# Kernel optimization log

Hardware: AMD Instinct MI355X
Metric: run time of the kernel (lower is better)

## Reference

```python
import jax, jax.numpy as jnp
import numpy as np
import math

V, T, D_POI, D_OUT = 200000, 512, 256, 512
D_IN = D_POI + 4
D_HID = D_POI + 100


def setup_inputs() -> dict:
    key = jax.random.key(0)
    ks = jax.random.split(key, 12)
    s = 0.02
    return {
        "prev_poi_idx": jax.random.randint(ks[0], (T,), 0, V),
        "prev_time_frac": jax.random.uniform(ks[1], (T,), jnp.float32),
        "poi_final_emb": jax.random.normal(ks[2], (V, D_POI), jnp.float32),
        "poi_latlon_deg": jax.random.uniform(ks[3], (V, 2), jnp.float32) * 90.0,
        "ln_w": jnp.ones((D_IN,), jnp.float32),
        "ln_b": jnp.zeros((D_IN,), jnp.float32),
        "w1": jax.random.normal(ks[4], (D_IN, D_HID), jnp.float32) * s,
        "b1": jnp.zeros((D_HID,), jnp.float32),
        "w2": jax.random.normal(ks[5], (D_HID, D_POI), jnp.float32) * s,
        "b2": jnp.zeros((D_POI,), jnp.float32),
        "w_ih": jax.random.normal(ks[6], (3 * D_OUT, D_POI), jnp.float32) * s,
        "w_hh": jax.random.normal(ks[7], (3 * D_OUT, D_OUT), jnp.float32) * s,
        "b_ih": jnp.zeros((3 * D_OUT,), jnp.float32),
        "b_hh": jnp.zeros((3 * D_OUT,), jnp.float32),
        "q": jax.random.normal(ks[8], (D_OUT,), jnp.float32),
        "log_lam": jnp.array(0.0, jnp.float32),  # log(recency_lambda=1.0)
    }


def _haversine_km(lat1, lon1, lat2, lon2, eps=1e-12):
    dlat = (lat2 - lat1) * 0.5
    dlon = (lon2 - lon1) * 0.5
    a = jnp.sin(dlat) ** 2 + jnp.clip(jnp.cos(lat1), -1, 1) * jnp.clip(jnp.cos(lat2), -1, 1) * jnp.sin(dlon) ** 2
    c = 2.0 * jnp.arctan2(jnp.sqrt(jnp.clip(a, 0, 1)), jnp.sqrt(jnp.clip(1 - a, eps, 1)))
    return 6371.0088 * c


def _forward(prev_poi_idx, prev_time_frac, poi_final_emb, poi_latlon_deg,
             ln_w, ln_b, w1, b1, w2, b2, w_ih, w_hh, b_ih, b_hh, q, log_lam):
    Tn = prev_poi_idx.shape[0]
    poi_emb = poi_final_emb[prev_poi_idx]                       # (T, d_poi)
    t = jnp.clip(prev_time_frac, 0.0, 1.0)
    sin_t = jnp.sin(2.0 * math.pi * t)
    cos_t = jnp.cos(2.0 * math.pi * t)
    dif = jnp.mod(t[1:] - t[:-1], 1.0) * 24.0
    dt_h = jnp.concatenate([jnp.zeros((1,), t.dtype), dif])
    # _poi_radians is under no_grad in torch
    latlon = jax.lax.stop_gradient(poi_latlon_deg[prev_poi_idx])
    lat = jnp.deg2rad(jnp.clip(latlon[:, 0], -90, 90))
    lon = jnp.deg2rad(jnp.clip(latlon[:, 1], -180, 180))
    dd = _haversine_km(lat[:-1], lon[:-1], lat[1:], lon[1:])
    dd_km = jnp.concatenate([jnp.zeros((1,), dd.dtype), dd])
    feat = jnp.stack([sin_t, cos_t, jnp.log1p(dt_h), jnp.log1p(dd_km)], axis=-1)  # (T, 4)
    x = jnp.concatenate([poi_emb, feat], axis=-1)               # (T, d_poi+4)
    # fuse: LayerNorm -> Linear -> GELU -> (Dropout eval=id) -> Linear
    mu = jnp.mean(x, axis=-1, keepdims=True)
    var = jnp.mean((x - mu) ** 2, axis=-1, keepdims=True)
    x = (x - mu) * jax.lax.rsqrt(var + 1e-5) * ln_w + ln_b
    x = jax.nn.gelu(x @ w1 + b1, approximate=False) @ w2 + b2   # (T, d_poi)
    # GRU (single layer, unidirectional), torch gate order r,z,n
    gi_all = x @ w_ih.T + b_ih                                  # (T, 3H)
    def step(h, gi):
        gh = h @ w_hh.T + b_hh
        gi_r, gi_z, gi_n = jnp.split(gi, 3)
        gh_r, gh_z, gh_n = jnp.split(gh, 3)
        r = jax.nn.sigmoid(gi_r + gh_r)
        z = jax.nn.sigmoid(gi_z + gh_z)
        n = jnp.tanh(gi_n + r * gh_n)
        h_new = (1.0 - z) * n + z * h
        return h_new, h_new
    h0 = jnp.zeros((D_OUT,), x.dtype)
    _, hs = jax.lax.scan(step, h0, gi_all)                      # (T, d_out)
    D = hs.shape[-1]
    score = hs @ (q[:D] / jnp.sqrt(jnp.asarray(D, hs.dtype)))
    age = jnp.arange(Tn, dtype=hs.dtype)
    lam = jnp.maximum(jnp.exp(log_lam), 1e-4)
    score = score - lam * (Tn - 1 - age)
    attn = jax.nn.softmax(score, axis=0)
    summary = jnp.sum(attn[:, None] * hs, axis=0, keepdims=True)  # (1, d_out)
    return summary, attn


def reference(prev_poi_idx, prev_time_frac, poi_final_emb, poi_latlon_deg,
              ln_w, ln_b, w1, b1, w2, b2, w_ih, w_hh, b_ih, b_hh, q, log_lam):
    return _forward(prev_poi_idx, prev_time_frac, poi_final_emb, poi_latlon_deg,
                    ln_w, ln_b, w1, b1, w2, b2, w_ih, w_hh, b_ih, b_hh, q, log_lam)
```

## Files before the change

### kernel.cpp

```cpp
#include <hip/hip_runtime.h>
#include <hip/hip_cooperative_groups.h>
#include <math.h>

namespace cg = cooperative_groups;

#define TT 512
#define DPOI 256
#define DIN 260
#define DHID 356
#define DOUTD 512
#define G3 1536

#define GB 32
#define HU (DOUTD / GB)
#define NR (3 * HU)

__global__ void feat_kernel(const int* __restrict__ idx, const float* __restrict__ timef,
                            const float* __restrict__ latlon, float* __restrict__ feat) {
    int i = threadIdx.x;
    if (i >= TT) return;
    float t = fminf(fmaxf(timef[i], 0.f), 1.f);
    const float TWO_PI = 6.28318530717958647692f;
    float s = sinf(TWO_PI * t);
    float c = cosf(TWO_PI * t);
    float dt_h = 0.f, dd = 0.f;
    if (i > 0) {
        float tp = fminf(fmaxf(timef[i - 1], 0.f), 1.f);
        float d = t - tp;
        d = d - floorf(d);
        dt_h = d * 24.f;
        int i0 = idx[i - 1], i1 = idx[i];
        float la0 = latlon[2 * (size_t)i0], lo0 = latlon[2 * (size_t)i0 + 1];
        float la1 = latlon[2 * (size_t)i1], lo1 = latlon[2 * (size_t)i1 + 1];
        const float D2R = 0.01745329251994329577f;
        float lat1 = fminf(fmaxf(la0, -90.f), 90.f) * D2R;
        float lon1 = fminf(fmaxf(lo0, -180.f), 180.f) * D2R;
        float lat2 = fminf(fmaxf(la1, -90.f), 90.f) * D2R;
        float lon2 = fminf(fmaxf(lo1, -180.f), 180.f) * D2R;
        float dlat = (lat2 - lat1) * 0.5f, dlon = (lon2 - lon1) * 0.5f;
        float sdlat = sinf(dlat), sdlon = sinf(dlon);
        float a = sdlat * sdlat +
                  fminf(fmaxf(cosf(lat1), -1.f), 1.f) * fminf(fmaxf(cosf(lat2), -1.f), 1.f) * sdlon * sdlon;
        float aa = fminf(fmaxf(a, 0.f), 1.f);
        float bb = fminf(fmaxf(1.f - a, 1e-12f), 1.f);
        float cc = 2.f * atan2f(sqrtf(aa), sqrtf(bb));
        dd = 6371.0088f * cc;
    }
    feat[4 * i + 0] = s;
    feat[4 * i + 1] = c;
    feat[4 * i + 2] = log1pf(dt_h);
    feat[4 * i + 3] = log1pf(dd);
}

__global__ void ln_kernel(const int* __restrict__ idx, const float* __restrict__ emb,
                          const float* __restrict__ feat, const float* __restrict__ lnw,
                          const float* __restrict__ lnb, float* __restrict__ xn) {
    int t = blockIdx.x;
    int tid = threadIdx.x;
    int wave = tid >> 6, lane = tid & 63;
    const float* row = emb + (size_t)idx[t] * DPOI;
    float v0 = row[tid];
    float v1 = (tid < 4) ? feat[4 * t + tid] : 0.f;

    __shared__ float red[4];
    __shared__ float mu_s, rs_s;

    float s = v0 + v1;
    for (int o = 32; o; o >>= 1) s += __shfl_down(s, o, 64);
    if (lane == 0) red[wave] = s;
    __syncthreads();
    if (tid == 0) mu_s = (red[0] + red[1] + red[2] + red[3]) * (1.f / 260.f);
    __syncthreads();
    float mu = mu_s;
    float d0 = v0 - mu;
    float d1 = (tid < 4) ? (v1 - mu) : 0.f;
    float sq = d0 * d0 + d1 * d1;
    for (int o = 32; o; o >>= 1) sq += __shfl_down(sq, o, 64);
    __syncthreads();
    if (lane == 0) red[wave] = sq;
    __syncthreads();
    if (tid == 0) {
        float var = (red[0] + red[1] + red[2] + red[3]) * (1.f / 260.f);
        rs_s = rsqrtf(var + 1e-5f);
    }
    __syncthreads();
    float rs = rs_s;
    xn[t * DIN + tid] = d0 * rs * lnw[tid] + lnb[tid];
    if (tid < 4)
        xn[t * DIN + 256 + tid] = d1 * rs * lnw[256 + tid] + lnb[256 + tid];
}

__global__ void mlp1_kernel(const float* __restrict__ xn, const float* __restrict__ w1,
                            const float* __restrict__ b1, float* __restrict__ h1) {
    int t = blockIdx.x, j = threadIdx.x;
    __shared__ float xl[DIN];
    for (int k = threadIdx.x; k < DIN; k += blockDim.x) xl[k] = xn[t * DIN + k];
    __syncthreads();
    if (j < DHID) {
        float acc = b1[j];
        #pragma unroll 4
        for (int k = 0; k < DIN; ++k) acc = fmaf(xl[k], w1[k * DHID + j], acc);
        float g = 0.5f * acc * (1.f + erff(acc * 0.70710678118654752440f));
        h1[t * DHID + j] = g;
    }
}

__global__ void mlp2_kernel(const float* __restrict__ h1, const float* __restrict__ w2,
                            const float* __restrict__ b2, float* __restrict__ x2) {
    int t = blockIdx.x, j = threadIdx.x;
    __shared__ float xl[DHID];
    for (int k = threadIdx.x; k < DHID; k += blockDim.x) xl[k] = h1[t * DHID + k];
    __syncthreads();
    float acc = b2[j];
    #pragma unroll 4
    for (int k = 0; k < DHID; ++k) acc = fmaf(xl[k], w2[k * DPOI + j], acc);
    x2[t * DPOI + j] = acc;
}

__global__ void gi_kernel(const float* __restrict__ x2, const float* __restrict__ wih,
                          const float* __restrict__ bih, float* __restrict__ gi) {
    int t = blockIdx.x;
    int tid = threadIdx.x;
    int wave = tid >> 6, lane = tid & 63;
    float4 xv = ((const float4*)(x2 + (size_t)t * DPOI))[lane];
    for (int r = wave; r < G3; r += 4) {
        float4 wv = ((const float4*)(wih + (size_t)r * DPOI))[lane];
        float s = xv.x * wv.x + xv.y * wv.y + xv.z * wv.z + xv.w * wv.w;
        for (int o = 32; o; o >>= 1) s += __shfl_down(s, o, 64);
        if (lane == 0) gi[(size_t)t * G3 + r] = s + bih[r];
    }
}

__global__ void zero_kernel(uint4* __restrict__ p, int n16) {
    int i = blockIdx.x * blockDim.x + threadIdx.x;
    int stride = gridDim.x * blockDim.x;
    uint4 z; z.x = 0u; z.y = 0u; z.z = 0u; z.w = 0u;
    for (; i < n16; i += stride) p[i] = z;
}

__global__ __launch_bounds__(1024)
void gru_tag_kernel(const float* __restrict__ gi, const float* __restrict__ whh,
                    const float* __restrict__ bhh, float* __restrict__ hs,
                    unsigned long long* __restrict__ hcomm) {
    __shared__ unsigned short w[NR][DOUTD];
    __shared__ float hprev[DOUTD];
    __shared__ float gsum[NR];
    __shared__ float bl[NR];

    int b = blockIdx.x;
    int tid = threadIdx.x;
    int wave = tid >> 6, lane = tid & 63;
    int jbase = b * HU;

    unsigned short* wl = &w[0][0];
    for (int e = tid; e < NR * DOUTD; e += 1024) {
        int rr = e >> 9, k = e & 511;
        int g = rr >> 4, jj = rr & 15;
        float v = whh[(size_t)(g * DOUTD + jbase + jj) * DOUTD + k];
        unsigned int u = __float_as_uint(v);
        u += 0x7fffu + ((u >> 16) & 1u);
        int kk = (k < 256) ? (((k >> 2) << 3) | (k & 3))
                           : ((((k - 256) >> 2) << 3) | 4 | (k & 3));
        wl[(rr << 9) + kk] = (unsigned short)(u >> 16);
    }
    if (tid < NR) {
        int g = tid >> 4, jj = tid & 15;
        bl[tid] = bhh[g * DOUTD + jbase + jj];
    }
    if (tid < DOUTD) hprev[tid] = 0.f;
    __syncthreads();

    const float4* hp4 = (const float4*)hprev;
    long budget = 2L * 1000 * 1000;

    float gir = 0.f, giz = 0.f, gin = 0.f, hreg = 0.f;
    if (tid < HU) {
        int j = jbase + tid;
        gir = gi[j];
        giz = gi[DOUTD + j];
        gin = gi[2 * DOUTD + j];
    }

    for (int s = 0; s < TT; ++s) {
        if (s > 0) {
            if (lane < 32) {
                int v = (wave << 5) + lane;
                bool own = (v >> 4) == b;
                const unsigned long long* ap = hcomm + (size_t)(s - 1) * DOUTD + v;
                unsigned long long p = 0;
                bool ok = own;
                while (!__all(ok)) {
                    if (!ok) {
                        p = __hip_atomic_load(ap, __ATOMIC_RELAXED,
                                              __HIP_MEMORY_SCOPE_AGENT);
                        ok = ((unsigned)(p >> 32) == (unsigned)s);
                    }
                    if (--budget < 0) break;
                }
                if (!own) hprev[v] = __uint_as_float((unsigned)p);
            }
            __syncthreads();
        }

        float4 ha = hp4[lane];
        float4 hb = hp4[64 + lane];
        #pragma unroll
        for (int rv = 0; rv < 3; ++rv) {
            int rr = wave * 3 + rv;
            uint4 wv = *(const uint4*)(wl + (rr << 9) + (lane << 3));
            float acc;
            acc = __uint_as_float(wv.x << 16) * ha.x;
            acc = fmaf(__uint_as_float(wv.x & 0xffff0000u), ha.y, acc);
            acc = fmaf(__uint_as_float(wv.y << 16), ha.z, acc);
            acc = fmaf(__uint_as_float(wv.y & 0xffff0000u), ha.w, acc);
            acc = fmaf(__uint_as_float(wv.z << 16), hb.x, acc);
            acc = fmaf(__uint_as_float(wv.z & 0xffff0000u), hb.y, acc);
            acc = fmaf(__uint_as_float(wv.w << 16), hb.z, acc);
            acc = fmaf(__uint_as_float(wv.w & 0xffff0000u), hb.w, acc);
            for (int o = 32; o; o >>= 1) acc += __shfl_down(acc, o, 64);
            if (lane == 0) gsum[rr] = acc + bl[rr];
        }
        __syncthreads();

        if (tid < HU) {
            int j = jbase + tid;
            float gr  = gir + gsum[tid];
            float gz  = giz + gsum[HU + tid];
            float ghn = gsum[2 * HU + tid];
            float r = 1.f / (1.f + expf(-gr));
            float z = 1.f / (1.f + expf(-gz));
            float n = tanhf(gin + r * ghn);
            float hn = (1.f - z) * n + z * hreg;
            hreg = hn;
            hs[(size_t)s * DOUTD + j] = hn;
            unsigned long long pay = ((unsigned long long)(unsigned)(s + 1) << 32) |
                                     (unsigned long long)__float_as_uint(hn);
            __hip_atomic_store(&hcomm[(size_t)s * DOUTD + j], pay,
                               __ATOMIC_RELAXED, __HIP_MEMORY_SCOPE_AGENT);
            hprev[j] = hn;
            if (s + 1 < TT) {
                const float* gn = gi + (size_t)(s + 1) * G3;
                gir = gn[j]; giz = gn[DOUTD + j]; gin = gn[2 * DOUTD + j];
            }
        }
    }
}

__global__ void attn_kernel(const float* __restrict__ hs, const float* __restrict__ q,
                            const float* __restrict__ log_lam, float* __restrict__ out) {
    int tid = threadIdx.x;
    int wave = tid >> 6, lane = tid & 63;
    __shared__ float sc[TT];
    __shared__ float at[TT];
    __shared__ float red[8];
    __shared__ float red2[8];
    __shared__ float denom_s, mx_s;

    const float qscale = 0.04419417382415921757f;
    for (int r = wave; r < TT; r += 8) {
        float acc = 0.f;
        #pragma unroll
        for (int m = 0; m < 8; ++m) {
            int k = lane + 64 * m;
            acc = fmaf(hs[(size_t)r * DOUTD + k], q[k], acc);
        }
        for (int o = 32; o; o >>= 1) acc += __shfl_down(acc, o, 64);
        if (lane == 0) sc[r] = acc * qscale;
    }
    __syncthreads();
    float lam = fmaxf(expf(log_lam[0]), 1e-4f);
    float s_i = sc[tid] - lam * (float)(TT - 1 - tid);

    float mval = s_i;
    for (int o = 32; o; o >>= 1) mval = fmaxf(mval, __shfl_down(mval, o, 64));
    if (lane == 0) red[wave] = mval;
    __syncthreads();
    if (tid == 0) {
        float mm = red[0];
        for (int i = 1; i < 8; ++i) mm = fmaxf(mm, red[i]);
        mx_s = mm;
    }
    __syncthreads();
    float e = expf(s_i - mx_s);
    float ssum = e;
    for (int o = 32; o; o >>= 1) ssum += __shfl_down(ssum, o, 64);
    if (lane == 0) red2[wave] = ssum;
    __syncthreads();
    if (tid == 0) {
        float dsum = 0.f;
        for (int i = 0; i < 8; ++i) dsum += red2[i];
        denom_s = dsum;
    }
    __syncthreads();
    float attn = e / denom_s;
    out[DOUTD + tid] = attn;
    at[tid] = attn;
    __syncthreads();
    float acc = 0.f;
    for (int i = 0; i < TT; ++i) acc = fmaf(at[i], hs[(size_t)i * DOUTD + tid], acc);
    out[tid] = acc;
}

extern "C" void kernel_launch(void* const* d_in, const int* in_sizes, int n_in,
                              void* d_out, int out_size, void* d_ws, size_t ws_size,
                              hipStream_t stream) {
    const int*   idx    = (const int*)d_in[0];
    const float* timef  = (const float*)d_in[1];
    const float* emb    = (const float*)d_in[2];
    const float* latlon = (const float*)d_in[3];
    const float* lnw    = (const float*)d_in[4];
    const float* lnb    = (const float*)d_in[5];
    const float* w1     = (const float*)d_in[6];
    const float* b1     = (const float*)d_in[7];
    const float* w2     = (const float*)d_in[8];
    const float* b2     = (const float*)d_in[9];
    const float* wih    = (const float*)d_in[10];
    const float* whh    = (const float*)d_in[11];
    const float* bih    = (const float*)d_in[12];
    const float* bhh    = (const float*)d_in[13];
    const float* q      = (const float*)d_in[14];
    const float* loglam = (const float*)d_in[15];
    float* out = (float*)d_out;

    unsigned long long* hcomm = (unsigned long long*)d_ws;
    float* feat = (float*)(hcomm + (size_t)TT * DOUTD);
    float* xn   = feat + 2048;
    float* h1   = xn + TT * DIN;
    float* x2   = h1 + TT * DHID;
    float* gi   = x2 + TT * DPOI;
    float* hs   = gi + (size_t)TT * G3;

    feat_kernel<<<1, TT, 0, stream>>>(idx, timef, latlon, feat);
    ln_kernel<<<TT, 256, 0, stream>>>(idx, emb, feat, lnw, lnb, xn);
    mlp1_kernel<<<TT, 384, 0, stream>>>(xn, w1, b1, h1);
    mlp2_kernel<<<TT, 256, 0, stream>>>(h1, w2, b2, x2);
    gi_kernel<<<TT, 256, 0, stream>>>(x2, wih, bih, gi);

    int n16 = (int)(((size_t)TT * DOUTD * 8) / 16);
    zero_kernel<<<256, 512, 0, stream>>>((uint4*)hcomm, n16);

    void* gru_args[] = { (void*)&gi, (void*)&whh, (void*)&bhh, (void*)&hs, (void*)&hcomm };
    hipLaunchCooperativeKernel((void*)gru_tag_kernel, dim3(GB), dim3(1024),
                               gru_args, 0, stream);

    attn_kernel<<<1, TT, 0, stream>>>(hs, q, loglam, out);
}
```

Before: 1.909 ms.

## Keep GRU recurrent weights in fp32 registers and pack two bf16 hidden values per flag

The W_hh slice each block owns now sits in fp32 registers instead of bf16 shared memory, so the conversion and unpacking work per step goes away, and the three row dot products are interleaved so they reduce together. The cross-block hidden-state exchange now packs two bf16-rounded hidden values with the step tag into each 64-bit atomic word. This halves the number of polled flags and the communication footprint. The cost is that neighbouring blocks see bf16-rounded hidden states while the owning block keeps fp32, which adds register pressure and slightly changes numerics.

```diff
diff --git a/kernel.cpp b/kernel.cpp
--- a/kernel.cpp
+++ b/kernel.cpp
@@ -14,6 +14,7 @@
 #define GB 32
 #define HU (DOUTD / GB)
 #define NR (3 * HU)
+#define NU 256
 
 __global__ void feat_kernel(const int* __restrict__ idx, const float* __restrict__ timef,
                             const float* __restrict__ latlon, float* __restrict__ feat) {
@@ -142,30 +143,30 @@
 void gru_tag_kernel(const float* __restrict__ gi, const float* __restrict__ whh,
                     const float* __restrict__ bhh, float* __restrict__ hs,
                     unsigned long long* __restrict__ hcomm) {
-    __shared__ unsigned short w[NR][DOUTD];
     __shared__ float hprev[DOUTD];
     __shared__ float gsum[NR];
-    __shared__ float bl[NR];
 
     int b = blockIdx.x;
     int tid = threadIdx.x;
     int wave = tid >> 6, lane = tid & 63;
     int jbase = b * HU;
 
-    unsigned short* wl = &w[0][0];
-    for (int e = tid; e < NR * DOUTD; e += 1024) {
-        int rr = e >> 9, k = e & 511;
-        int g = rr >> 4, jj = rr & 15;
-        float v = whh[(size_t)(g * DOUTD + jbase + jj) * DOUTD + k];
-        unsigned int u = __float_as_uint(v);
-        u += 0x7fffu + ((u >> 16) & 1u);
-        int kk = (k < 256) ? (((k >> 2) << 3) | (k & 3))
-                           : ((((k - 256) >> 2) << 3) | 4 | (k & 3));
-        wl[(rr << 9) + kk] = (unsigned short)(u >> 16);
-    }
-    if (tid < NR) {
-        int g = tid >> 4, jj = tid & 15;
-        bl[tid] = bhh[g * DOUTD + jbase + jj];
+    float4 wa0, wb0, wa1, wb1, wa2, wb2;
+    float bl0, bl1, bl2;
+    {
+        int rr = wave * 3;
+        int g0 = (rr + 0) >> 4, j0 = (rr + 0) & 15;
+        int g1 = (rr + 1) >> 4, j1 = (rr + 1) & 15;
+        int g2 = (rr + 2) >> 4, j2 = (rr + 2) & 15;
+        const float4* r0 = (const float4*)(whh + (size_t)(g0 * DOUTD + jbase + j0) * DOUTD);
+        const float4* r1 = (const float4*)(whh + (size_t)(g1 * DOUTD + jbase + j1) * DOUTD);
+        const float4* r2 = (const float4*)(whh + (size_t)(g2 * DOUTD + jbase + j2) * DOUTD);
+        wa0 = r0[lane]; wb0 = r0[64 + lane];
+        wa1 = r1[lane]; wb1 = r1[64 + lane];
+        wa2 = r2[lane]; wb2 = r2[64 + lane];
+        bl0 = bhh[g0 * DOUTD + jbase + j0];
+        bl1 = bhh[g1 * DOUTD + jbase + j1];
+        bl2 = bhh[g2 * DOUTD + jbase + j2];
     }
     if (tid < DOUTD) hprev[tid] = 0.f;
     __syncthreads();
@@ -183,42 +184,52 @@
 
     for (int s = 0; s < TT; ++s) {
         if (s > 0) {
-            if (lane < 32) {
-                int v = (wave << 5) + lane;
-                bool own = (v >> 4) == b;
-                const unsigned long long* ap = hcomm + (size_t)(s - 1) * DOUTD + v;
+            if (lane < 16) {
+                int u = (wave << 4) + lane;
+                bool own = (u >> 3) == b;
+                const unsigned long long* ap = hcomm + (size_t)(s - 1) * NU + u;
                 unsigned long long p = 0;
                 bool ok = own;
                 while (!__all(ok)) {
                     if (!ok) {
                         p = __hip_atomic_load(ap, __ATOMIC_RELAXED,
                                               __HIP_MEMORY_SCOPE_AGENT);
-                        ok = ((unsigned)(p >> 32) == (unsigned)s);
+                        ok = ((unsigned)p == (unsigned)s);
                     }
                     if (--budget < 0) break;
                 }
-                if (!own) hprev[v] = __uint_as_float((unsigned)p);
+                if (!own) {
+                    unsigned hi = (unsigned)(p >> 32);
+                    float2 hv;
+                    hv.x = __uint_as_float(hi & 0xffff0000u);
+                    hv.y = __uint_as_float(hi << 16);
+                    *(float2*)&hprev[2 * u] = hv;
+                }
             }
             __syncthreads();
         }
 
         float4 ha = hp4[lane];
         float4 hb = hp4[64 + lane];
-        #pragma unroll
-        for (int rv = 0; rv < 3; ++rv) {
-            int rr = wave * 3 + rv;
-            uint4 wv = *(const uint4*)(wl + (rr << 9) + (lane << 3));
-            float acc;
-            acc = __uint_as_float(wv.x << 16) * ha.x;
-            acc = fmaf(__uint_as_float(wv.x & 0xffff0000u), ha.y, acc);
-            acc = fmaf(__uint_as_float(wv.y << 16), ha.z, acc);
-            acc = fmaf(__uint_as_float(wv.y & 0xffff0000u), ha.w, acc);
-            acc = fmaf(__uint_as_float(wv.z << 16), hb.x, acc);
-            acc = fmaf(__uint_as_float(wv.z & 0xffff0000u), hb.y, acc);
-            acc = fmaf(__uint_as_float(wv.w << 16), hb.z, acc);
-            acc = fmaf(__uint_as_float(wv.w & 0xffff0000u), hb.w, acc);
-            for (int o = 32; o; o >>= 1) acc += __shfl_down(acc, o, 64);
-            if (lane == 0) gsum[rr] = acc + bl[rr];
+        float a0, a1, a2;
+        a0 = wa0.x * ha.x; a1 = wa1.x * ha.x; a2 = wa2.x * ha.x;
+        a0 = fmaf(wa0.y, ha.y, a0); a1 = fmaf(wa1.y, ha.y, a1); a2 = fmaf(wa2.y, ha.y, a2);
+        a0 = fmaf(wa0.z, ha.z, a0); a1 = fmaf(wa1.z, ha.z, a1); a2 = fmaf(wa2.z, ha.z, a2);
+        a0 = fmaf(wa0.w, ha.w, a0); a1 = fmaf(wa1.w, ha.w, a1); a2 = fmaf(wa2.w, ha.w, a2);
+        a0 = fmaf(wb0.x, hb.x, a0); a1 = fmaf(wb1.x, hb.x, a1); a2 = fmaf(wb2.x, hb.x, a2);
+        a0 = fmaf(wb0.y, hb.y, a0); a1 = fmaf(wb1.y, hb.y, a1); a2 = fmaf(wb2.y, hb.y, a2);
+        a0 = fmaf(wb0.z, hb.z, a0); a1 = fmaf(wb1.z, hb.z, a1); a2 = fmaf(wb2.z, hb.z, a2);
+        a0 = fmaf(wb0.w, hb.w, a0); a1 = fmaf(wb1.w, hb.w, a1); a2 = fmaf(wb2.w, hb.w, a2);
+        for (int o = 32; o; o >>= 1) {
+            a0 += __shfl_down(a0, o, 64);
+            a1 += __shfl_down(a1, o, 64);
+            a2 += __shfl_down(a2, o, 64);
+        }
+        if (lane == 0) {
+            int rr = wave * 3;
+            gsum[rr]     = a0 + bl0;
+            gsum[rr + 1] = a1 + bl1;
+            gsum[rr + 2] = a2 + bl2;
         }
         __syncthreads();
 
@@ -232,11 +243,18 @@
             float n = tanhf(gin + r * ghn);
             float hn = (1.f - z) * n + z * hreg;
             hreg = hn;
+            unsigned ub = __float_as_uint(hn);
+            ub += 0x7fffu + ((ub >> 16) & 1u);
+            unsigned bh = ub >> 16;
+            unsigned p0 = (unsigned)__shfl((int)bh, (tid & 7) * 2, 64);
+            unsigned p1 = (unsigned)__shfl((int)bh, (tid & 7) * 2 + 1, 64);
+            if (tid < 8) {
+                unsigned long long pay = ((unsigned long long)((p0 << 16) | p1) << 32) |
+                                         (unsigned)(s + 1);
+                __hip_atomic_store(&hcomm[(size_t)s * NU + b * 8 + tid], pay,
+                                   __ATOMIC_RELAXED, __HIP_MEMORY_SCOPE_AGENT);
+            }
             hs[(size_t)s * DOUTD + j] = hn;
-            unsigned long long pay = ((unsigned long long)(unsigned)(s + 1) << 32) |
-                                     (unsigned long long)__float_as_uint(hn);
-            __hip_atomic_store(&hcomm[(size_t)s * DOUTD + j], pay,
-                               __ATOMIC_RELAXED, __HIP_MEMORY_SCOPE_AGENT);
             hprev[j] = hn;
             if (s + 1 < TT) {
                 const float* gn = gi + (size_t)(s + 1) * G3;
@@ -323,7 +341,7 @@
     float* out = (float*)d_out;
 
     unsigned long long* hcomm = (unsigned long long*)d_ws;
-    float* feat = (float*)(hcomm + (size_t)TT * DOUTD);
+    float* feat = (float*)(hcomm + (size_t)TT * NU);
     float* xn   = feat + 2048;
     float* h1   = xn + TT * DIN;
     float* x2   = h1 + TT * DHID;
@@ -336,7 +354,7 @@
     mlp2_kernel<<<TT, 256, 0, stream>>>(h1, w2, b2, x2);
     gi_kernel<<<TT, 256, 0, stream>>>(x2, wih, bih, gi);
 
-    int n16 = (int)(((size_t)TT * DOUTD * 8) / 16);
+    int n16 = (int)(((size_t)TT * NU * 8) / 16);
     zero_kernel<<<256, 512, 0, stream>>>((uint4*)hcomm, n16);
 
     void* gru_args[] = { (void*)&gi, (void*)&whh, (void*)&bhh, (void*)&hs, (void*)&hcomm };
```

Measured after the change: 1.885 ms. No clear change (-1.2%).
